# Performance work log

Hardware: AMD Instinct MI355X
Metric: run time of the kernel (lower is better)

Reference implementation:

```python
import jax, jax.numpy as jnp
import numpy as np

MARGIN = 1.0
EPS = 1e-12


def setup_inputs() -> dict:
    key = jax.random.key(0)
    k1, k2, k3 = jax.random.split(key, 3)
    B, C, D = 16384, 500, 512
    features = jax.random.normal(k1, (B, D), dtype=jnp.float32)
    prototypes = jax.random.normal(k2, (C, D), dtype=jnp.float32)
    labels = jax.random.randint(k3, (B,), 0, C, dtype=jnp.int64)
    return {"features": features, "prototypes": prototypes, "labels": labels}


def reference(features, prototypes, labels):
    # Pairwise L2 distances [B, C] via the expanded form (no [B,C,D] intermediate)
    f2 = jnp.sum(features * features, axis=-1, keepdims=True)   # [B, 1]
    p2 = jnp.sum(prototypes * prototypes, axis=-1)               # [C]
    sq = f2 + p2 - 2.0 * (features @ prototypes.T)               # [B, C]
    dists = jnp.sqrt(jnp.maximum(sq, EPS))                       # [B, C]

    B, C = dists.shape
    d_pos = jnp.take_along_axis(dists, labels[:, None], axis=1)[:, 0]  # [B]
    pos_mask = jax.nn.one_hot(labels, C, dtype=bool)             # [B, C]
    d_neg_min = jnp.min(jnp.where(pos_mask, jnp.inf, dists), axis=-1)  # [B]

    loss = jnp.mean(jax.nn.relu(d_pos - d_neg_min + MARGIN))
    return loss
```

## Files before the change

### kernel.cpp

```cpp
#include <hip/hip_runtime.h>
#include <stdint.h>
#include <stddef.h>

#define BB 16384
#define CC 500
#define DD 512
#define PADC 512
#define LMARGIN 1.0f
#define EPSQ 1e-12f
#define NK 16

typedef __attribute__((ext_vector_type(8))) _Float16 f16x8;
typedef __attribute__((ext_vector_type(4))) _Float16 f16x4;
typedef __attribute__((ext_vector_type(4))) float f32x4;

__global__ void prepP_kernel(const float* __restrict__ protos,
                             unsigned short* __restrict__ protoT,
                             float* __restrict__ p2,
                             float* __restrict__ out) {
  __shared__ float s_arr[16][17];
  const int cg = blockIdx.x;
  const int t = threadIdx.x;
  const int colin = t & 15;
  const int jb = t >> 4;
  const int col = cg * 16 + colin;
  if (cg == 0 && t == 0) out[0] = 0.f;
  float s = 0.f;
#pragma unroll
  for (int u = 0; u < 4; ++u) {
    const int j8 = jb + u * 16;
    const int kc = j8 >> 2, quad = j8 & 3;
    f32x4 a0 = {0.f, 0.f, 0.f, 0.f}, a1 = a0;
    if (col < CC) {
      const float* src = protos + (size_t)col * DD + j8 * 8;
      a0 = *(const f32x4*)src;
      a1 = *(const f32x4*)(src + 4);
    }
    f16x8 h;
#pragma unroll
    for (int uu = 0; uu < 4; ++uu) {
      h[uu] = (_Float16)a0[uu];
      h[uu + 4] = (_Float16)a1[uu];
      s = fmaf(a0[uu], a0[uu], s);
      s = fmaf(a1[uu], a1[uu], s);
    }
    *(f16x8*)(protoT + (size_t)(cg * 16 + kc) * 512 + (quad * 16 + colin) * 8) = h;
  }
  s_arr[colin][jb] = s;
  __syncthreads();
  if (t < 16) {
    float acc = 0.f;
#pragma unroll
    for (int i = 0; i < 16; ++i) acc += s_arr[t][i];
    p2[cg * 16 + t] = acc;
  }
}

__launch_bounds__(512, 2)
__global__ void main_kernel(const float* __restrict__ feat,
                            const unsigned short* __restrict__ protoT,
                            const float* __restrict__ p2,
                            const int* __restrict__ labels,
                            float* __restrict__ out) {
  __shared__ __align__(16) unsigned char Ab[3][4096];
  __shared__ float f2l[64];

  const int tid = threadIdx.x;
  const int w = tid >> 6;
  const int lane = tid & 63;
  const int lane16 = lane & 15;
  const int quad = lane >> 4;
  const int r0 = blockIdx.x * 64;

  float* redM = (float*)&Ab[1][0];
  float* redP = (float*)&Ab[1][2048];

  const int arow = tid >> 3;
  const int aj = tid & 7;
  const float* aSrc = feat + (size_t)(r0 + arow) * DD + aj * 4;
  const int awoff = arow * 64 + (((aj >> 1) ^ ((arow >> 1) & 3)) * 16) + (aj & 1) * 8;
  const int aroff = lane16 * 64 + ((quad ^ ((lane16 >> 1) & 3)) * 16);

  const char* bptr[4];
#pragma unroll
  for (int nt = 0; nt < 4; ++nt)
    bptr[nt] = (const char*)protoT + (size_t)((w * 4 + nt) * 16) * 1024 + lane * 16;

  f32x4 acc[4][4];
#pragma unroll
  for (int mt = 0; mt < 4; ++mt)
#pragma unroll
    for (int nt = 0; nt < 4; ++nt) acc[mt][nt] = (f32x4){0.f, 0.f, 0.f, 0.f};

  float f2acc = 0.f;
  f16x8 bfr[3][4];
  f32x4 aC;

  {
    f32x4 a0 = *(const f32x4*)(aSrc);
    f32x4 a1 = *(const f32x4*)(aSrc + 32);
    aC = *(const f32x4*)(aSrc + 64);
#pragma unroll
    for (int nt = 0; nt < 4; ++nt) {
      bfr[0][nt] = *(const f16x8*)(bptr[nt]);
      bfr[1][nt] = *(const f16x8*)(bptr[nt] + 1024);
    }
    f16x4 h0, h1;
#pragma unroll
    for (int u = 0; u < 4; ++u) {
      h0[u] = (_Float16)a0[u];
      h1[u] = (_Float16)a1[u];
      f2acc = fmaf(a0[u], a0[u], f2acc);
      f2acc = fmaf(a1[u], a1[u], f2acc);
    }
    *(f16x4*)(&Ab[0][awoff]) = h0;
    *(f16x4*)(&Ab[1][awoff]) = h1;
  }
  __syncthreads();

#pragma unroll
  for (int kc = 0; kc < NK; ++kc) {
    f32x4 aN;
    if (kc + 3 < NK) aN = *(const f32x4*)(aSrc + (kc + 3) * 32);
    if (kc + 2 < NK) {
#pragma unroll
      for (int nt = 0; nt < 4; ++nt)
        bfr[(kc + 2) % 3][nt] = *(const f16x8*)(bptr[nt] + (kc + 2) * 1024);
    }

    f16x8 af[4];
#pragma unroll
    for (int mt = 0; mt < 4; ++mt)
      af[mt] = *(const f16x8*)(&Ab[kc % 3][mt * 1024 + aroff]);
#pragma unroll
    for (int mt = 0; mt < 4; ++mt)
#pragma unroll
      for (int nt = 0; nt < 4; ++nt)
        acc[mt][nt] = __builtin_amdgcn_mfma_f32_16x16x32_f16(
            af[mt], bfr[kc % 3][nt], acc[mt][nt], 0, 0, 0);

    if (kc + 2 < NK) {
      f16x4 h;
#pragma unroll
      for (int u = 0; u < 4; ++u) {
        h[u] = (_Float16)aC[u];
        f2acc = fmaf(aC[u], aC[u], f2acc);
      }
      *(f16x4*)(&Ab[(kc + 2) % 3][awoff]) = h;
      aC = aN;
    }
    __syncthreads();
  }

  f2acc += __shfl_xor(f2acc, 1, 64);
  f2acc += __shfl_xor(f2acc, 2, 64);
  f2acc += __shfl_xor(f2acc, 4, 64);
  if ((tid & 7) == 0) f2l[arow] = f2acc;

  float p2v[4];
#pragma unroll
  for (int nt = 0; nt < 4; ++nt) p2v[nt] = p2[w * 64 + nt * 16 + lane16];

#pragma unroll
  for (int mt = 0; mt < 4; ++mt) {
#pragma unroll
    for (int i = 0; i < 4; ++i) {
      const int row = mt * 16 + quad * 4 + i;
      const int lb = labels[r0 + row];
      float qm = 1e30f, qp = -1e30f;
#pragma unroll
      for (int nt = 0; nt < 4; ++nt) {
        const int col = w * 64 + nt * 16 + lane16;
        float q = p2v[nt] - 2.f * acc[mt][nt][i];
        bool isPos = (col == lb);
        qp = fmaxf(qp, isPos ? q : -1e30f);
        qm = fminf(qm, (!isPos && col < CC) ? q : 1e30f);
      }
#pragma unroll
      for (int d = 1; d < 16; d <<= 1) {
        qm = fminf(qm, __shfl_xor(qm, d, 64));
        qp = fmaxf(qp, __shfl_xor(qp, d, 64));
      }
      if (lane16 == 0) {
        redM[row * 8 + w] = qm;
        redP[row * 8 + w] = qp;
      }
    }
  }
  __syncthreads();

  if (tid < 64) {
    float qm = 1e30f, qp = -1e30f;
#pragma unroll
    for (int j = 0; j < 8; ++j) {
      qm = fminf(qm, redM[tid * 8 + j]);
      qp = fmaxf(qp, redP[tid * 8 + j]);
    }
    float f2 = f2l[tid];
    float dn = sqrtf(fmaxf(f2 + qm, EPSQ));
    float dp = sqrtf(fmaxf(f2 + qp, EPSQ));
    float term = fmaxf(dp - dn + LMARGIN, 0.f);
#pragma unroll
    for (int d = 1; d < 64; d <<= 1) term += __shfl_xor(term, d, 64);
    if (tid == 0) atomicAdd(out, term * (1.0f / BB));
  }
}

extern "C" void kernel_launch(void* const* d_in, const int* in_sizes, int n_in,
                              void* d_out, int out_size, void* d_ws, size_t ws_size,
                              hipStream_t stream) {
  const float* feat = (const float*)d_in[0];
  const float* protos = (const float*)d_in[1];
  const int* labels = (const int*)d_in[2];
  float* out = (float*)d_out;

  char* ws = (char*)d_ws;
  unsigned short* protoT = (unsigned short*)(ws);
  float* p2 = (float*)(ws + (512 << 10));

  prepP_kernel<<<32, 256, 0, stream>>>(protos, protoT, p2, out);
  main_kernel<<<BB / 64, 512, 0, stream>>>(feat, protoT, p2, labels, out);
}
```

Measured before the change: 93.62 us.

## Stage full feature tile in LDS upfront and drop per-chunk barriers

Instead of a 3-deep rotating LDS ring for the feature tile with a barrier after every K chunk, all 16 feature chunks are loaded, converted to fp16 and written to LDS once before the MFMA loop, which then runs with no synchronisation. p2 and labels are also staged in LDS, and the reduction buffers get their own space. This removes 16 block-wide barriers and the interleaved conversion work, but raises LDS use to about 64KB per block, which may cut occupancy below the two blocks per CU the launch bounds ask for. It also serialises all global feature loads ahead of any compute.

```diff
diff --git a/kernel.cpp b/kernel.cpp
--- a/kernel.cpp
+++ b/kernel.cpp
@@ -62,8 +62,11 @@
                             const float* __restrict__ p2,
                             const int* __restrict__ labels,
                             float* __restrict__ out) {
-  __shared__ __align__(16) unsigned char Ab[3][4096];
+  __shared__ __align__(16) unsigned char Afull[NK * 4096];
+  __shared__ float p2l[PADC];
   __shared__ float f2l[64];
+  __shared__ int labl[64];
+  __shared__ float redM[64 * 8], redP[64 * 8];
 
   const int tid = threadIdx.x;
   const int w = tid >> 6;
@@ -72,101 +75,98 @@
   const int quad = lane >> 4;
   const int r0 = blockIdx.x * 64;
 
-  float* redM = (float*)&Ab[1][0];
-  float* redP = (float*)&Ab[1][2048];
+  const char* bptr[4];
+#pragma unroll
+  for (int nt = 0; nt < 4; ++nt)
+    bptr[nt] = (const char*)protoT + (size_t)(w * 64 + nt * 16) * 1024 + lane * 16;
+
+  f16x8 bfr[3][4];
+#pragma unroll
+  for (int nt = 0; nt < 4; ++nt) {
+    bfr[0][nt] = *(const f16x8*)(bptr[nt]);
+    bfr[1][nt] = *(const f16x8*)(bptr[nt] + 1024);
+  }
 
   const int arow = tid >> 3;
   const int aj = tid & 7;
   const float* aSrc = feat + (size_t)(r0 + arow) * DD + aj * 4;
-  const int awoff = arow * 64 + (((aj >> 1) ^ ((arow >> 1) & 3)) * 16) + (aj & 1) * 8;
+  const int awbase =
+      arow * 64 + (((aj >> 1) ^ ((arow >> 1) & 3)) * 16) + (aj & 1) * 8;
+
+  float s = 0.f;
+  {
+    f32x4 av0[8], av1[8];
+#pragma unroll
+    for (int i = 0; i < 8; ++i) av0[i] = *(const f32x4*)(aSrc + i * 32);
+#pragma unroll
+    for (int i = 0; i < 8; ++i) av1[i] = *(const f32x4*)(aSrc + (8 + i) * 32);
+#pragma unroll
+    for (int i = 0; i < 8; ++i) {
+      f16x4 h;
+#pragma unroll
+      for (int u = 0; u < 4; ++u) {
+        h[u] = (_Float16)av0[i][u];
+        s = fmaf(av0[i][u], av0[i][u], s);
+      }
+      *(f16x4*)(&Afull[i * 4096 + awbase]) = h;
+    }
+#pragma unroll
+    for (int i = 0; i < 8; ++i) {
+      f16x4 h;
+#pragma unroll
+      for (int u = 0; u < 4; ++u) {
+        h[u] = (_Float16)av1[i][u];
+        s = fmaf(av1[i][u], av1[i][u], s);
+      }
+      *(f16x4*)(&Afull[(8 + i) * 4096 + awbase]) = h;
+    }
+  }
+  s += __shfl_xor(s, 1, 64);
+  s += __shfl_xor(s, 2, 64);
+  s += __shfl_xor(s, 4, 64);
+  if ((lane & 7) == 0) f2l[arow] = s;
+
+  p2l[tid] = p2[tid];
+  if (tid < 64) labl[tid] = labels[r0 + tid];
+
+  f32x4 acc[4][4];
+#pragma unroll
+  for (int mt = 0; mt < 4; ++mt)
+#pragma unroll
+    for (int nt = 0; nt < 4; ++nt) acc[mt][nt] = (f32x4){0.f, 0.f, 0.f, 0.f};
+
+  __syncthreads();
+
   const int aroff = lane16 * 64 + ((quad ^ ((lane16 >> 1) & 3)) * 16);
-
-  const char* bptr[4];
-#pragma unroll
-  for (int nt = 0; nt < 4; ++nt)
-    bptr[nt] = (const char*)protoT + (size_t)((w * 4 + nt) * 16) * 1024 + lane * 16;
-
-  f32x4 acc[4][4];
-#pragma unroll
-  for (int mt = 0; mt < 4; ++mt)
-#pragma unroll
-    for (int nt = 0; nt < 4; ++nt) acc[mt][nt] = (f32x4){0.f, 0.f, 0.f, 0.f};
-
-  float f2acc = 0.f;
-  f16x8 bfr[3][4];
-  f32x4 aC;
-
-  {
-    f32x4 a0 = *(const f32x4*)(aSrc);
-    f32x4 a1 = *(const f32x4*)(aSrc + 32);
-    aC = *(const f32x4*)(aSrc + 64);
-#pragma unroll
-    for (int nt = 0; nt < 4; ++nt) {
-      bfr[0][nt] = *(const f16x8*)(bptr[nt]);
-      bfr[1][nt] = *(const f16x8*)(bptr[nt] + 1024);
-    }
-    f16x4 h0, h1;
-#pragma unroll
-    for (int u = 0; u < 4; ++u) {
-      h0[u] = (_Float16)a0[u];
-      h1[u] = (_Float16)a1[u];
-      f2acc = fmaf(a0[u], a0[u], f2acc);
-      f2acc = fmaf(a1[u], a1[u], f2acc);
-    }
-    *(f16x4*)(&Ab[0][awoff]) = h0;
-    *(f16x4*)(&Ab[1][awoff]) = h1;
-  }
-  __syncthreads();
-
 #pragma unroll
   for (int kc = 0; kc < NK; ++kc) {
-    f32x4 aN;
-    if (kc + 3 < NK) aN = *(const f32x4*)(aSrc + (kc + 3) * 32);
     if (kc + 2 < NK) {
 #pragma unroll
       for (int nt = 0; nt < 4; ++nt)
         bfr[(kc + 2) % 3][nt] = *(const f16x8*)(bptr[nt] + (kc + 2) * 1024);
     }
-
     f16x8 af[4];
 #pragma unroll
     for (int mt = 0; mt < 4; ++mt)
-      af[mt] = *(const f16x8*)(&Ab[kc % 3][mt * 1024 + aroff]);
+      af[mt] = *(const f16x8*)(&Afull[kc * 4096 + mt * 1024 + aroff]);
 #pragma unroll
     for (int mt = 0; mt < 4; ++mt)
 #pragma unroll
       for (int nt = 0; nt < 4; ++nt)
         acc[mt][nt] = __builtin_amdgcn_mfma_f32_16x16x32_f16(
             af[mt], bfr[kc % 3][nt], acc[mt][nt], 0, 0, 0);
-
-    if (kc + 2 < NK) {
-      f16x4 h;
-#pragma unroll
-      for (int u = 0; u < 4; ++u) {
-        h[u] = (_Float16)aC[u];
-        f2acc = fmaf(aC[u], aC[u], f2acc);
-      }
-      *(f16x4*)(&Ab[(kc + 2) % 3][awoff]) = h;
-      aC = aN;
-    }
-    __syncthreads();
-  }
-
-  f2acc += __shfl_xor(f2acc, 1, 64);
-  f2acc += __shfl_xor(f2acc, 2, 64);
-  f2acc += __shfl_xor(f2acc, 4, 64);
-  if ((tid & 7) == 0) f2l[arow] = f2acc;
+  }
 
   float p2v[4];
 #pragma unroll
-  for (int nt = 0; nt < 4; ++nt) p2v[nt] = p2[w * 64 + nt * 16 + lane16];
+  for (int nt = 0; nt < 4; ++nt) p2v[nt] = p2l[w * 64 + nt * 16 + lane16];
 
 #pragma unroll
   for (int mt = 0; mt < 4; ++mt) {
 #pragma unroll
     for (int i = 0; i < 4; ++i) {
       const int row = mt * 16 + quad * 4 + i;
-      const int lb = labels[r0 + row];
+      const int lb = labl[row];
       float qm = 1e30f, qp = -1e30f;
 #pragma unroll
       for (int nt = 0; nt < 4; ++nt) {
```

After: 93.13 us. About the same (-0.5%).
